# Optimization experiments

Measured on AMD Instinct MI355X. Metric: run time of the kernel, lower is better.

## Reference

```python
import jax, jax.numpy as jnp
import numpy as np

IN_DIM = 1024
FF = 512
OUT = 128
TEMP = 1.0  # temperature=1 passed in __init__
EPS = 1e-5  # BatchNorm3d eps


def make_pe(n, d):
    # PositionalEncoding table, rows 0..n-1
    pos = jnp.arange(n, dtype=jnp.float32)[:, None]
    div = jnp.exp(jnp.arange(0, d, 2, dtype=jnp.float32) * (-np.log(10000.0) / d))
    ang = pos * div  # [n, d/2]
    return jnp.stack([jnp.sin(ang), jnp.cos(ang)], axis=-1).reshape(n, d)


def _nonlocal(x, kw, qw, vw, ow, ob, g, beta):
    # x: [B, C, T, H, W]; 1x1x1 convs are channel matmuls
    B, C, T, H, W = x.shape
    K = jnp.einsum('bcthw,fc->bfthw', x, kw).reshape(B, FF, -1)
    Q = jnp.einsum('bcthw,fc->bfthw', x, qw).reshape(B, FF, -1)
    V = jnp.einsum('bcthw,fc->bfthw', x, vw).reshape(B, FF, -1)
    KQ = jnp.einsum('bcn,bcm->bnm', K, Q)  # K^T Q over channels -> [B,N,N]
    attn = jax.nn.softmax(KQ / TEMP, axis=2)
    # torch: sum_j V[b,c,n] * attn[b,n,j]  == V * attn.sum(axis=2)
    Vo = (V * attn.sum(axis=2)[:, None, :]).reshape(B, FF, T, H, W)
    o = jnp.einsum('bfthw,of->bothw', Vo, ow) + ob[None, :, None, None, None]
    y = x + jax.nn.relu(o)
    # BatchNorm3d, training-mode batch statistics over (B,T,H,W)
    m = y.mean(axis=(0, 2, 3, 4))
    v = y.var(axis=(0, 2, 3, 4))
    inv = jax.lax.rsqrt(v + EPS)
    return ((y - m[None, :, None, None, None]) * inv[None, :, None, None, None]
            * g[None, :, None, None, None] + beta[None, :, None, None, None])


def _convt2(x, w, b):
    # ConvTranspose2d(kernel=2, stride=2): each input pixel emits a 2x2 block
    B, C, H, W = x.shape
    y = jnp.einsum('bchw,cokl->bohkwl', x, w).reshape(B, w.shape[1], 2 * H, 2 * W)
    return y + b[None, :, None, None]


def setup_inputs() -> dict:
    key = jax.random.key(0)
    ks = jax.random.split(key, 32)
    n = lambda k, s, sc: jax.random.normal(k, s, dtype=jnp.float32) * sc
    d = {
        'context': n(ks[0], (4, 4, IN_DIM, 16, 16), 1.0),
        'frame': n(ks[1], (4, 6, IN_DIM, 8, 8), 1.0),
    }
    i = 2
    for l in (0, 1):
        d[f'nl{l}_kw'] = n(ks[i], (FF, IN_DIM), IN_DIM ** -0.5); i += 1
        d[f'nl{l}_qw'] = n(ks[i], (FF, IN_DIM), IN_DIM ** -0.5); i += 1
        d[f'nl{l}_vw'] = n(ks[i], (FF, IN_DIM), IN_DIM ** -0.5); i += 1
        d[f'nl{l}_ow'] = n(ks[i], (IN_DIM, FF), FF ** -0.5); i += 1
        d[f'nl{l}_ob'] = n(ks[i], (IN_DIM,), 0.02); i += 1
        d[f'nl{l}_g'] = jnp.ones((IN_DIM,), jnp.float32)
        d[f'nl{l}_beta'] = jnp.zeros((IN_DIM,), jnp.float32)
    d['tp_w'] = n(ks[i], (FF, IN_DIM, 3, 3, 3), (IN_DIM * 27) ** -0.5); i += 1
    d['tp_b'] = n(ks[i], (FF,), 0.02); i += 1
    d['up1_w'] = n(ks[i], (IN_DIM, FF, 2, 2), IN_DIM ** -0.5); i += 1
    d['up1_b'] = n(ks[i], (FF,), 0.02); i += 1
    d['up2_w'] = n(ks[i], (FF, FF, 2, 2), FF ** -0.5); i += 1
    d['up2_b'] = n(ks[i], (FF,), 0.02); i += 1
    for p in ('og', 'os'):
        d[f'{p}1_w'] = n(ks[i], (FF, FF), FF ** -0.5); i += 1
        d[f'{p}1_b'] = n(ks[i], (FF,), 0.02); i += 1
        d[f'{p}2_w'] = n(ks[i], (OUT, FF), FF ** -0.5); i += 1
        d[f'{p}2_b'] = n(ks[i], (OUT,), 0.02); i += 1
    return d


def reference(context, frame,
              nl0_kw, nl0_qw, nl0_vw, nl0_ow, nl0_ob, nl0_g, nl0_beta,
              nl1_kw, nl1_qw, nl1_vw, nl1_ow, nl1_ob, nl1_g, nl1_beta,
              tp_w, tp_b, up1_w, up1_b, up2_w, up2_b,
              og1_w, og1_b, og2_w, og2_b, os1_w, os1_b, os2_w, os2_b):
    # context: [B, Tc, C, H, W] -> [B, C, Tc, H, W]
    x = jnp.transpose(context, (0, 2, 1, 3, 4))
    x = _nonlocal(x, nl0_kw, nl0_qw, nl0_vw, nl0_ow, nl0_ob, nl0_g, nl0_beta)
    x = _nonlocal(x, nl1_kw, nl1_qw, nl1_vw, nl1_ow, nl1_ob, nl1_g, nl1_beta)
    # temporal pool: Conv3d kernel 3, VALID, then ReLU and global avg pool
    tp = jax.lax.conv_general_dilated(x, tp_w, (1, 1, 1), 'VALID',
                                      dimension_numbers=('NCDHW', 'OIDHW', 'NCDHW'))
    tp = jax.nn.relu(tp + tp_b[None, :, None, None, None])
    goal_pre = tp.mean(axis=(2, 3, 4))  # [B, FF]
    B, T, C, H, W = frame.shape
    f = frame.reshape(B * T, C, H, W)
    s = jax.nn.relu(_convt2(f, up1_w, up1_b))
    s = _convt2(s, up2_w, up2_b)  # [B*T, FF, 4H, 4W]
    Ns = 16 * H * W
    se = s.reshape(B * T, FF, Ns)
    pe = make_pe(Ns, FF)
    Vt = jnp.transpose(se, (0, 2, 1)) + pe[None]  # [B*T, Ns, FF]
    goal_rep = jnp.repeat(goal_pre, T, axis=0)  # [B*T, FF]
    SG = jnp.einsum('bcn,bc->bn', se, goal_rep)
    attn = jax.nn.softmax(SG / TEMP, axis=1)
    sga = jnp.einsum('bn,bnc->bc', attn, Vt).reshape(B, T, FF)
    goal = jax.nn.relu(goal_pre @ og1_w.T + og1_b) @ og2_w.T + og2_b
    state = jax.nn.relu(sga @ os1_w.T + os1_b) @ os2_w.T + os2_b
    return goal, state
```

## Files before the change

kernel.cpp:

```cpp
#include <hip/hip_runtime.h>
#include <hip/hip_bf16.h>

using bf16 = __hip_bfloat16;
typedef short short8 __attribute__((ext_vector_type(8)));
typedef float float4v __attribute__((ext_vector_type(4)));

__device__ __forceinline__ float b2f(unsigned short u){
  unsigned int x = ((unsigned int)u) << 16; float f;
  __builtin_memcpy(&f, &x, 4); return f;
}
__device__ __forceinline__ float b2f(bf16 v){ return __bfloat162float(v); }
__device__ __forceinline__ unsigned short f2bu(float x){
  bf16 h = __float2bfloat16(x); unsigned short u;
  __builtin_memcpy(&u, &h, 2); return u;
}

#define GLDS16(g, l) __builtin_amdgcn_global_load_lds( \
    (const __attribute__((address_space(1))) void*)(g), \
    (__attribute__((address_space(3))) void*)(l), 16, 0, 0)

template<int N> __device__ __forceinline__ void vwait(){
  if constexpr (N==0)       asm volatile("s_waitcnt vmcnt(0)" ::: "memory");
  else if constexpr (N==3)  asm volatile("s_waitcnt vmcnt(3)" ::: "memory");
  else if constexpr (N==4)  asm volatile("s_waitcnt vmcnt(4)" ::: "memory");
  else if constexpr (N==5)  asm volatile("s_waitcnt vmcnt(5)" ::: "memory");
  else if constexpr (N==6)  asm volatile("s_waitcnt vmcnt(6)" ::: "memory");
  else if constexpr (N==8)  asm volatile("s_waitcnt vmcnt(8)" ::: "memory");
  else if constexpr (N==10) asm volatile("s_waitcnt vmcnt(10)" ::: "memory");
  else                      asm volatile("s_waitcnt vmcnt(12)" ::: "memory");
}

template<class TO>
__launch_bounds__(256)
__global__ void permT_k(const float* __restrict__ inp, TO* __restrict__ outp,
                        int Cc, int R, int D, int G, long inS, long outS){
  __shared__ float t[64][65];
  int z = blockIdx.z;
  const float* in = inp + (size_t)z*inS;
  TO* out = outp + (size_t)z*outS;
  int c0 = blockIdx.x*64, r0 = blockIdx.y*64;
  int tid = threadIdx.x;
  int rr = tid>>2, c4 = (tid&3)*16;
  const float* p = in + (size_t)(r0+rr)*Cc + c0 + c4;
  #pragma unroll
  for (int j=0;j<16;j+=4){
    float4 q = *reinterpret_cast<const float4*>(p+j);
    t[rr][c4+j]=q.x; t[rr][c4+j+1]=q.y; t[rr][c4+j+2]=q.z; t[rr][c4+j+3]=q.w;
  }
  __syncthreads();
  int ql = tid>>2;
  int q = c0 + ql;
  int orow = (q % D)*G + q / D;
  TO* op = out + (size_t)orow*R + r0 + c4;
  #pragma unroll
  for (int j=0;j<16;j++){
    if constexpr (sizeof(TO)==2) op[j] = __float2bfloat16(t[c4+j][ql]);
    else op[j] = t[c4+j][ql];
  }
}

template<int PAT>
__launch_bounds__(256)
__global__ void permTsplit3_k(const float* __restrict__ inp, unsigned short* __restrict__ outp,
                              int Cc, int R, int D, int G, long inS, long outS){
  __shared__ float t[64][65];
  int z = blockIdx.z;
  const float* in = inp + (size_t)z*inS;
  unsigned short* out = outp + (size_t)z*outS;
  int c0 = blockIdx.x*64, r0 = blockIdx.y*64;
  int tid = threadIdx.x;
  int rr = tid>>2, c4 = (tid&3)*16;
  const float* p = in + (size_t)(r0+rr)*Cc + c0 + c4;
  #pragma unroll
  for (int j=0;j<16;j+=4){
    float4 q = *reinterpret_cast<const float4*>(p+j);
    t[rr][c4+j]=q.x; t[rr][c4+j+1]=q.y; t[rr][c4+j+2]=q.z; t[rr][c4+j+3]=q.w;
  }
  __syncthreads();
  int ql = tid>>2;
  int q = c0 + ql;
  int orow = (q % D)*G + q / D;
  unsigned short* op = out + (size_t)orow*(3*R);
  #pragma unroll
  for (int j=0;j<16;j++){
    float v = t[c4+j][ql];
    unsigned short h = f2bu(v);
    unsigned short l = f2bu(v - b2f(h));
    int idx = r0 + c4 + j;
    if constexpr (PAT==0){
      op[idx] = h; op[R+idx] = l; op[2*R+idx] = h;
    } else {
      op[idx] = h; op[R+idx] = h; op[2*R+idx] = l;
    }
  }
}

__launch_bounds__(256)
__global__ void splitA_k(const float* __restrict__ in, unsigned short* __restrict__ out){
  int idx = blockIdx.x*256 + threadIdx.x;
  int m = idx >> 9, j = idx & 511;
  float v = in[idx];
  unsigned short h = f2bu(v);
  unsigned short l = f2bu(v - b2f(h));
  unsigned short* op = out + (size_t)m*1536 + j;
  op[0] = h; op[512] = l; op[1024] = h;
}

__global__ void zero_k(float* __restrict__ p){
  p[blockIdx.x*256 + threadIdx.x] = 0.f;
}

template<int WM, int WN, int MTM, int NTN, int MODE, int BK>
__launch_bounds__(256)
__global__ void mmL_k(const unsigned short* __restrict__ A,
                      const unsigned short* __restrict__ B,
                      const float* __restrict__ bias,
                      const unsigned short* __restrict__ res,
                      const float* __restrict__ gpf,
                      float* __restrict__ outf,
                      unsigned short* __restrict__ outs,
                      float* __restrict__ aux,
                      int K){
  constexpr int BM  = WM*MTM*16;
  constexpr int BN  = WN*NTN*16;
  constexpr int CPR = BK/8;
  constexpr int KS  = BK/32;
  constexpr int AIT = (BM*CPR)/256;
  constexpr int NBC = (BN*CPR)/256;
  constexpr int LPT = AIT + NBC;
  __shared__ __align__(16) short As[3*BM*BK];
  __shared__ __align__(16) short Bs[3*BN*BK];
  const int tid = threadIdx.x;
  const int wv = tid>>6, lane = tid&63, l15 = lane&15, quad = lane>>4;
  const int wvm = wv / WN, wvf = wv % WN;
  const int wbase = wv<<6;

  int bx = blockIdx.x, by = blockIdx.y, bz = blockIdx.z;
  if constexpr (MODE==1){
    const int gx = gridDim.x, gy = gridDim.y, gz = gridDim.z;
    const int n = gx*gy*gz;
    const int lin = bx + gx*(by + gy*bz);
    const int q = n >> 3, r = n & 7;
    const int xcd = lin & 7, j = lin >> 3;
    const int work = (xcd < r ? xcd*(q+1) : r*(q+1) + (xcd-r)*q) + j;
    by = work % gy;
    const int t = work / gy;
    bx = t % gx;
    bz = t / gx;
  }
  const int m0 = bx*BM;
  const int fblk = by*BN;
  const int z = bz;

  auto swz = [](int row){ if constexpr (BK==32) return (row>>1)&3; else return row&7; };

  size_t aAddr[AIT];
  #pragma unroll
  for (int it=0; it<AIT; ++it){
    int s = tid + it*256;
    int arow = s/CPR;
    int ac = (s&(CPR-1)) ^ swz(arow);
    int m = m0 + arow;
    if constexpr (MODE==1){
      int mm = m < 1568 ? m : 1567;
      int b = mm/392, r = mm%392;
      int t = r/196, r2 = r%196;
      int hh = r2/14, ww = r2%14;
      int kt = z/3, kh = z%3;
      int sp = ((b*4 + t + kt)*16 + hh + kh)*16 + ww;
      aAddr[it] = (size_t)sp*1024 + ac*8;
    } else {
      aAddr[it] = (size_t)m*K + ac*8;
    }
  }
  size_t bAddr[NBC];
  #pragma unroll
  for (int it=0; it<NBC; ++it){
    int s = tid + it*256;
    int row = s/CPR;
    int c = (s&(CPR-1)) ^ swz(row);
    int f = fblk + row;
    if constexpr (MODE==0)      bAddr[it] = (size_t)f*1024 + c*8;
    else if constexpr (MODE==1) bAddr[it] = (size_t)f*27648 + (size_t)z*3072 + c*8;
    else                        bAddr[it] = ((size_t)z*512 + f)*(size_t)K + c*8;
  }
  int aslot[MTM][KS];
  #pragma unroll
  for (int mt=0;mt<MTM;++mt)
    #pragma unroll
    for (int ks=0;ks<KS;++ks){
      int row = wvm*MTM*16 + mt*16 + l15;
      aslot[mt][ks] = row*CPR + ((ks*4 + quad) ^ swz(row));
    }
  int bslot[NTN][KS];
  #pragma unroll
  for (int nt=0;nt<NTN;++nt)
    #pragma unroll
    for (int ks=0;ks<KS;++ks){
      int row = wvf*NTN*16 + nt*16 + l15;
      bslot[nt][ks] = row*CPR + ((ks*4 + quad) ^ swz(row));
    }

  float4v acc[MTM][NTN];
  #pragma unroll
  for (int i=0;i<MTM;i++)
    #pragma unroll
    for (int j=0;j<NTN;j++) acc[i][j]=(float4v){0,0,0,0};

  auto stage = [&](int buf, int k0){
    #pragma unroll
    for (int it=0; it<AIT; ++it)
      GLDS16(A + aAddr[it] + k0, As + buf*(BM*BK) + (it*256 + wbase)*8);
    #pragma unroll
    for (int it=0; it<NBC; ++it)
      GLDS16(B + bAddr[it] + k0, Bs + buf*(BN*BK) + (it*256 + wbase)*8);
  };
  auto computeTile = [&](int buf){
    const short* ap = As + buf*(BM*BK);
    const short* bp = Bs + buf*(BN*BK);
    #pragma unroll
    for (int ks=0; ks<KS; ++ks){
      short8 bf[NTN];
      #pragma unroll
      for (int nt=0;nt<NTN;++nt)
        bf[nt] = *reinterpret_cast<const short8*>(bp + bslot[nt][ks]*8);
      #pragma unroll
      for (int mt=0;mt<MTM;++mt){
        short8 af = *reinterpret_cast<const short8*>(ap + aslot[mt][ks]*8);
        #pragma unroll
        for (int nt=0;nt<NTN;++nt)
          acc[mt][nt] = __builtin_amdgcn_mfma_f32_16x16x32_bf16(af, bf[nt], acc[mt][nt],0,0,0);
      }
    }
  };

  const int nt = K/BK;
  int b0=0, b1=1, b2=2;
  stage(b0, 0);
  for (int t=0; t<nt-1; ++t){
    stage(b1, (t+1)*BK);
    vwait<LPT>();
    __builtin_amdgcn_sched_barrier(0);
    __builtin_amdgcn_s_barrier();
    __builtin_amdgcn_sched_barrier(0);
    computeTile(b0);
    int tmp=b0; b0=b1; b1=b2; b2=tmp;
  }
  vwait<0>();
  __builtin_amdgcn_sched_barrier(0);
  __builtin_amdgcn_s_barrier();
  __builtin_amdgcn_sched_barrier(0);
  computeTile(b0);

  if constexpr (MODE==0){
    const float* badd = outf;
    float sacc[NTN] = {}, s2acc[NTN] = {};
    #pragma unroll
    for (int nt2=0;nt2<NTN;++nt2){
      int f = fblk + wvf*NTN*16 + nt2*16 + l15;
      float bi = bias[f] + (badd ? badd[f] : 0.f);
      float rsc = 1.f, rsh = 0.f;
      if (gpf){ rsc = gpf[f]; rsh = gpf[1024+f]; }
      #pragma unroll
      for (int mt=0;mt<MTM;++mt){
        #pragma unroll
        for (int r=0;r<4;++r){
          int m = m0 + wvm*MTM*16 + mt*16 + quad*4 + r;
          float v = fmaxf(acc[mt][nt2][r]+bi, 0.f) + b2f(res[(size_t)m*1024 + f])*rsc + rsh;
          outs[(size_t)m*1024 + f] = f2bu(v);
          sacc[nt2] += v; s2acc[nt2] += v*v;
        }
      }
    }
    #pragma unroll
    for (int nt2=0;nt2<NTN;++nt2){
      float s = sacc[nt2], s2 = s2acc[nt2];
      s  += __shfl_xor(s, 16);  s  += __shfl_xor(s, 32);
      s2 += __shfl_xor(s2, 16); s2 += __shfl_xor(s2, 32);
      if (quad==0){
        int f = fblk + wvf*NTN*16 + nt2*16 + l15;
        aux[(size_t)bx*2048 + f] = s;
        aux[(size_t)bx*2048 + 1024 + f] = s2;
      }
    }
  } else if constexpr (MODE==1){
    #pragma unroll
    for (int mt=0;mt<MTM;++mt)
      #pragma unroll
      for (int nt2=0;nt2<NTN;++nt2){
        int f = fblk + wvf*NTN*16 + nt2*16 + l15;
        #pragma unroll
        for (int r=0;r<4;++r){
          int m = m0 + wvm*MTM*16 + mt*16 + quad*4 + r;
          if (m < 1568) outf[((size_t)z*1568 + m)*512 + f] = acc[mt][nt2][r];
        }
      }
  } else if constexpr (MODE==2){
    int kk = z>>1, ll = z&1;
    #pragma unroll
    for (int mt=0;mt<MTM;++mt)
      #pragma unroll
      for (int nt2=0;nt2<NTN;++nt2){
        int f = fblk + wvf*NTN*16 + nt2*16 + l15;
        float bi = bias[f];
        #pragma unroll
        for (int r=0;r<4;++r){
          int m = m0 + wvm*MTM*16 + mt*16 + quad*4 + r;
          int bt = m>>6, p = m&63;
          long orow = (long)bt*256 + (2*(p>>3)+kk)*16 + 2*(p&7)+ll;
          float v = fmaxf(acc[mt][nt2][r]+bi, 0.f);
          unsigned short h = f2bu(v);
          unsigned short l = f2bu(v - b2f(h));
          unsigned short* rp = outs + (size_t)orow*1536 + f;
          rp[0] = h; rp[512] = l; rp[1024] = h;
        }
      }
  } else if constexpr (MODE==5){
    int kk = z>>1, ll = z&1;
    #pragma unroll
    for (int mt=0;mt<MTM;++mt){
      int mbase = m0 + wvm*MTM*16 + mt*16;
      int bt = mbase>>8, b6 = bt/6, p0 = mbase&255;
      float gv[NTN], bv[NTN];
      #pragma unroll
      for (int nt2=0;nt2<NTN;++nt2){
        int f = fblk + wvf*NTN*16 + nt2*16 + l15;
        gv[nt2] = gpf[b6*512 + f];
        bv[nt2] = bias[f];
      }
      #pragma unroll
      for (int r=0;r<4;++r){
        int p = p0 + quad*4 + r;
        long orow = (long)bt*1024 + (2*(p>>4)+kk)*32 + 2*(p&15)+ll;
        float sdot = 0.f;
        #pragma unroll
        for (int nt2=0;nt2<NTN;++nt2){
          int f = fblk + wvf*NTN*16 + nt2*16 + l15;
          float v = acc[mt][nt2][r] + bv[nt2];
          outf[(size_t)orow*512 + f] = v;
          sdot += v * gv[nt2];
        }
        sdot += __shfl_xor(sdot, 1); sdot += __shfl_xor(sdot, 2);
        sdot += __shfl_xor(sdot, 4); sdot += __shfl_xor(sdot, 8);
        if (l15==0) atomicAdd(aux + orow, sdot);
      }
    }
  } else {
    if (gpf){
      float sc[NTN], sh[NTN];
      #pragma unroll
      for (int nt2=0;nt2<NTN;++nt2){
        int f = fblk + wvf*NTN*16 + nt2*16 + l15;
        sc[nt2] = gpf[f]; sh[nt2] = gpf[1024+f];
      }
      #pragma unroll
      for (int mt=0;mt<MTM;++mt){
        #pragma unroll
        for (int r=0;r<4;++r){
          int m = m0 + wvm*MTM*16 + mt*16 + quad*4 + r;
          float part = 0.f;
          #pragma unroll
          for (int nt2=0;nt2<NTN;++nt2){
            int f = fblk + wvf*NTN*16 + nt2*16 + l15;
            float a = acc[mt][nt2][r];
            part += a * sh[nt2];
            outs[(size_t)m*1024 + f] = f2bu(a * sc[nt2]);
          }
          part += __shfl_xor(part, 1); part += __shfl_xor(part, 2);
          part += __shfl_xor(part, 4); part += __shfl_xor(part, 8);
          if (l15==0) atomicAdd(aux + m, part);
        }
      }
    } else {
      #pragma unroll
      for (int mt=0;mt<MTM;++mt)
        #pragma unroll
        for (int nt2=0;nt2<NTN;++nt2){
          int f = fblk + wvf*NTN*16 + nt2*16 + l15;
          #pragma unroll
          for (int r=0;r<4;++r){
            int m = m0 + wvm*MTM*16 + mt*16 + quad*4 + r;
            outs[(size_t)m*1024 + f] = f2bu(acc[mt][nt2][r]);
          }
        }
    }
  }
}

__global__ void stats_comb(const float* __restrict__ bnp, const float* __restrict__ g,
                           const float* __restrict__ beta, float* __restrict__ mv){
  int c = blockIdx.x*256 + threadIdx.x;
  float S=0.f, S2=0.f;
  #pragma unroll 8
  for (int s=0;s<64;s++){ S += bnp[(size_t)s*2048 + c]; S2 += bnp[(size_t)s*2048 + 1024 + c]; }
  float m = S * (1.f/4096.f);
  float var = S2 * (1.f/4096.f) - m*m;
  float inv = rsqrtf(var + 1e-5f);
  float sc = inv * g[c];
  mv[c] = sc;
  mv[1024 + c] = beta[c] - m*sc;
}

__launch_bounds__(256)
__global__ void wperm_k(const float* __restrict__ w, const float* __restrict__ mv1,
                        unsigned short* __restrict__ wtt, float* __restrict__ tpb2){
  __shared__ float ls[3456];
  __shared__ float rs[256];
  int f = blockIdx.x, cc = blockIdx.y;
  const float* src = w + (size_t)f*27648 + cc*3456;
  unsigned short* dst = wtt + (size_t)f*27648;
  for (int i=threadIdx.x; i<3456; i+=256) ls[i] = src[i];
  __syncthreads();
  float part = 0.f;
  for (int u=threadIdx.x; u<3456; u+=256){
    int j = u >> 7, c = u & 127;
    int ch = cc*128 + c;
    float wv = ls[c*27 + j];
    dst[(size_t)j*1024 + ch] = f2bu(wv * mv1[ch]);
    part += wv * mv1[1024 + ch];
  }
  rs[threadIdx.x] = part; __syncthreads();
  for (int st=128; st>0; st>>=1){
    if (threadIdx.x < st) rs[threadIdx.x] += rs[threadIdx.x+st];
    __syncthreads();
  }
  if (threadIdx.x==0) atomicAdd(tpb2 + f, rs[0]);
}

__launch_bounds__(256)
__global__ void gp2_k(const float* __restrict__ part9, const float* __restrict__ tpb,
                      const float* __restrict__ tpbA, float* __restrict__ gp){
  int b = blockIdx.x;
  int fc = blockIdx.y;
  int z = blockIdx.z;
  int fi = threadIdx.x & 31, pi = threadIdx.x >> 5;
  int f = fc*32 + fi;
  float bias = tpb[f] + tpbA[f];
  float a = 0.f;
  for (int p = z*49 + pi; p < z*49 + 49; p += 8){
    size_t base = ((size_t)(b*392 + p))*512 + f;
    float v = bias;
    #pragma unroll
    for (int i=0;i<9;i++) v += part9[(size_t)i*802816 + base];
    a += fmaxf(v, 0.f);
  }
  __shared__ float red[256];
  red[threadIdx.x] = a; __syncthreads();
  for (int st=4; st>0; st>>=1){
    if (pi < st) red[pi*32+fi] += red[(pi+st)*32+fi];
    __syncthreads();
  }
  if (pi==0) atomicAdd(gp + b*512 + f, red[fi] * (1.f/392.f));
}

__global__ void pen_k(float* __restrict__ peN){
  int idx = blockIdx.x*256 + threadIdx.x;
  int n = idx >> 9, c = idx & 511;
  float div = expf(-0.035977892f * (float)(c>>1));
  float ang = (float)n * div;
  peN[idx] = (c & 1) ? cosf(ang) : sinf(ang);
}

__launch_bounds__(256)
__global__ void softmax_k(const float* __restrict__ SG, float* __restrict__ attn){
  int bt = blockIdx.x; int tid = threadIdx.x;
  float4 v = *reinterpret_cast<const float4*>(SG + bt*1024 + tid*4);
  float mx = fmaxf(fmaxf(v.x,v.y), fmaxf(v.z,v.w));
  __shared__ float red[256];
  red[tid] = mx; __syncthreads();
  for (int st=128; st>0; st>>=1){
    if (tid<st) red[tid] = fmaxf(red[tid], red[tid+st]);
    __syncthreads();
  }
  float m = red[0]; __syncthreads();
  float4 e;
  e.x = expf(v.x-m); e.y = expf(v.y-m); e.z = expf(v.z-m); e.w = expf(v.w-m);
  red[tid] = e.x+e.y+e.z+e.w; __syncthreads();
  for (int st=128; st>0; st>>=1){
    if (tid<st) red[tid] += red[tid+st];
    __syncthreads();
  }
  float inv = 1.0f/red[0];
  e.x*=inv; e.y*=inv; e.z*=inv; e.w*=inv;
  *reinterpret_cast<float4*>(attn + bt*1024 + tid*4) = e;
}

__launch_bounds__(256)
__global__ void sga2_k(const float* __restrict__ scl, const float* __restrict__ peN,
                       const float* __restrict__ attn, float* __restrict__ sga){
  int bt = blockIdx.x, sl = blockIdx.y;
  int tid = threadIdx.x;
  __shared__ float at[32];
  if (tid < 32) at[tid] = attn[bt*1024 + sl*32 + tid];
  __syncthreads();
  float acc0 = 0.f, acc1 = 0.f;
  for (int j=0;j<32;j++){
    int n = sl*32 + j;
    float a = at[j];
    const float* row = scl + ((size_t)bt*1024 + n)*512;
    const float* pe  = peN + (size_t)n*512;
    acc0 += a * (row[tid] + pe[tid]);
    acc1 += a * (row[tid+256] + pe[tid+256]);
  }
  atomicAdd(sga + (size_t)bt*512 + tid, acc0);
  atomicAdd(sga + (size_t)bt*512 + 256 + tid, acc1);
}

__launch_bounds__(256)
__global__ void mlp_k(const float* __restrict__ in, const float* __restrict__ w1,
                      const float* __restrict__ b1, const float* __restrict__ w2,
                      const float* __restrict__ b2, float* __restrict__ out){
  int bb = blockIdx.x; int tid = threadIdx.x;
  __shared__ float xv[512]; __shared__ float h[512];
  xv[tid] = in[(size_t)bb*512 + tid];
  xv[tid+256] = in[(size_t)bb*512 + 256 + tid];
  __syncthreads();
  #pragma unroll
  for (int oo=0;oo<2;oo++){
    int o = tid + oo*256;
    const float* wr = w1 + (size_t)o*512;
    float a=0.f;
    for (int c=0;c<512;c+=4){
      float4 q = *reinterpret_cast<const float4*>(wr+c);
      a += xv[c]*q.x + xv[c+1]*q.y + xv[c+2]*q.z + xv[c+3]*q.w;
    }
    h[o] = fmaxf(a + b1[o], 0.f);
  }
  __syncthreads();
  if (tid < 128){
    const float* wr = w2 + (size_t)tid*512;
    float a=0.f;
    for (int c=0;c<512;c+=4){
      float4 q = *reinterpret_cast<const float4*>(wr+c);
      a += h[c]*q.x + h[c+1]*q.y + h[c+2]*q.z + h[c+3]*q.w;
    }
    out[(size_t)bb*128+tid] = a + b2[tid];
  }
}

extern "C" void kernel_launch(void* const* d_in, const int* in_sizes, int n_in,
                              void* d_out, int out_size, void* d_ws, size_t ws_size,
                              hipStream_t stream){
  (void)in_sizes; (void)n_in; (void)out_size; (void)ws_size;
  const float* ctx   = (const float*)d_in[0];
  const float* frame = (const float*)d_in[1];
  const float* nl_vw[2] = {(const float*)d_in[4],  (const float*)d_in[11]};
  const float* nl_ow[2] = {(const float*)d_in[5],  (const float*)d_in[12]};
  const float* nl_ob[2] = {(const float*)d_in[6],  (const float*)d_in[13]};
  const float* nl_g[2]  = {(const float*)d_in[7],  (const float*)d_in[14]};
  const float* nl_be[2] = {(const float*)d_in[8],  (const float*)d_in[15]};
  const float* tp_w = (const float*)d_in[16]; const float* tp_b = (const float*)d_in[17];
  const float* up1w = (const float*)d_in[18]; const float* up1b = (const float*)d_in[19];
  const float* up2w = (const float*)d_in[20]; const float* up2b = (const float*)d_in[21];
  const float* og1w = (const float*)d_in[22]; const float* og1b = (const float*)d_in[23];
  const float* og2w = (const float*)d_in[24]; const float* og2b = (const float*)d_in[25];
  const float* os1w = (const float*)d_in[26]; const float* os1b = (const float*)d_in[27];
  const float* os2w = (const float*)d_in[28]; const float* os2b = (const float*)d_in[29];
  float* out = (float*)d_out;

  char* wsp = (char*)d_ws;
  float* bias2   = (float*)(wsp + 65536);
  float* tpb2    = (float*)(wsp + 69632);
  float* gp      = (float*)(wsp + 73728);
  float* mv0     = (float*)(wsp + 131072);
  float* mv1     = (float*)(wsp + 139264);
  float* SG      = (float*)(wsp + 147456);
  float* attn    = (float*)(wsp + 245760);
  float* sga     = (float*)(wsp + 344064);
  float* peN     = (float*)(wsp + 786432);
  bf16*  weff    = (bf16*) (wsp + 2883584);
  unsigned short* w1sp = (unsigned short*)(wsp + 4980736);
  unsigned short* w2sp = (unsigned short*)(wsp + 17563648);
  char* ov = wsp + 23855104;
  bf16*  xclA = (bf16*) (ov);
  bf16*  xclB = (bf16*) (ov + 8388608);
  unsigned short* Asp = (unsigned short*)(ov + 36700160);
  unsigned short* Bsp = (unsigned short*)(ov + 36700160 + 3145728);
  float* bnp = (float*)(ov + 36700160 + 6291456);
  unsigned short* wtt = (unsigned short*)(ov + 8388608);
  float* part9 = (float*)(ov + 36700160);
  unsigned short* Fsp = (unsigned short*)(ov + 36700160);
  unsigned short* s1sp = (unsigned short*)(ov);
  float* scl  = (float*)(ov + 18874368);

  permT_k<bf16><<<dim3(4,16,16),256,0,stream>>>(ctx, xclA, 256, 1024, 1, 1, 262144L, 262144L);
  permTsplit3_k<1><<<dim3(32,16,1),256,0,stream>>>(up1w, w1sp, 2048, 1024, 4, 512, 0L, 0L);
  permTsplit3_k<1><<<dim3(32,8,1),256,0,stream>>>(up2w, w2sp, 2048, 512, 4, 512, 0L, 0L);
  pen_k<<<2048,256,0,stream>>>(peN);
  zero_k<<<320,256,0,stream>>>((float*)(wsp + 65536));

  splitA_k<<<2048,256,0,stream>>>(nl_ow[0], Asp);
  permTsplit3_k<1><<<dim3(16,8,1),256,0,stream>>>(nl_vw[0], Bsp, 1024, 512, 1, 1, 0L, 0L);
  mmL_k<1,4,2,2,4,64><<<dim3(32,8,1),256,0,stream>>>(Asp, Bsp, nullptr, nullptr, nullptr,
      nullptr, (unsigned short*)weff, nullptr, 1536);
  mmL_k<1,4,4,2,0,64><<<dim3(64,8,1),256,0,stream>>>((const unsigned short*)xclA,
      (const unsigned short*)weff, nl_ob[0], (const unsigned short*)xclA, nullptr,
      nullptr, (unsigned short*)xclB, bnp, 1024);
  stats_comb<<<4,256,0,stream>>>(bnp, nl_g[0], nl_be[0], mv0);

  splitA_k<<<2048,256,0,stream>>>(nl_ow[1], Asp);
  permTsplit3_k<1><<<dim3(16,8,1),256,0,stream>>>(nl_vw[1], Bsp, 1024, 512, 1, 1, 0L, 0L);
  mmL_k<1,4,2,2,4,64><<<dim3(32,8,1),256,0,stream>>>(Asp, Bsp, nullptr, nullptr, mv0,
      nullptr, (unsigned short*)weff, bias2, 1536);
  mmL_k<1,4,4,2,0,64><<<dim3(64,8,1),256,0,stream>>>((const unsigned short*)xclB,
      (const unsigned short*)weff, nl_ob[1], (const unsigned short*)xclB, mv0,
      bias2, (unsigned short*)xclA, bnp, 1024);
  stats_comb<<<4,256,0,stream>>>(bnp, nl_g[1], nl_be[1], mv1);

  wperm_k<<<dim3(512,8),256,0,stream>>>(tp_w, mv1, wtt, tpb2);
  mmL_k<2,2,4,4,1,32><<<dim3(13,4,9),256,0,stream>>>((const unsigned short*)xclA, wtt,
      nullptr, nullptr, nullptr, part9, nullptr, nullptr, 3072);
  gp2_k<<<dim3(4,16,8),256,0,stream>>>(part9, tp_b, tpb2, gp);

  permTsplit3_k<0><<<dim3(1,16,24),256,0,stream>>>(frame, Fsp, 64, 1024, 1, 1, 65536L, 196608L);
  mmL_k<1,4,4,2,2,64><<<dim3(24,4,4),256,0,stream>>>(Fsp, w1sp, up1b, nullptr, nullptr,
      nullptr, s1sp, nullptr, 3072);
  mmL_k<2,2,4,4,5,32><<<dim3(48,4,4),256,0,stream>>>(s1sp, w2sp, up2b, nullptr, gp,
      scl, nullptr, SG, 1536);

  softmax_k<<<24,256,0,stream>>>(SG, attn);
  sga2_k<<<dim3(24,32),256,0,stream>>>(scl, peN, attn, sga);

  mlp_k<<<4,256,0,stream>>>(gp, og1w, og1b, og2w, og2b, out);
  mlp_k<<<24,256,0,stream>>>(sga, os1w, os1b, os2w, os2b, out + 512);
}
```

Measured before the change: 602.8 us.

## Merge prep kernels into combined launches and add 4-buffer pipeline for temporal-pool GEMM

Five independent preprocessing launches (context transpose, two upconv weight splits, positional encoding, zeroing) are merged into one prep kernel that dispatches on block index. The per-layer splitA and value-weight split are merged into one layerprep kernel. This cuts launch overhead and idle gaps between small kernels. The temporal-pool GEMM also gets a 4-buffer LDS pipeline with prefetch distance two, in place of the 3-buffer scheme, to hide more load latency. The cost is more shared memory per block, which may lower occupancy.

```diff
diff --git a/kernel.cpp b/kernel.cpp
--- a/kernel.cpp
+++ b/kernel.cpp
@@ -30,16 +30,12 @@
   else                      asm volatile("s_waitcnt vmcnt(12)" ::: "memory");
 }
 
-template<class TO>
-__launch_bounds__(256)
-__global__ void permT_k(const float* __restrict__ inp, TO* __restrict__ outp,
-                        int Cc, int R, int D, int G, long inS, long outS){
-  __shared__ float t[64][65];
-  int z = blockIdx.z;
-  const float* in = inp + (size_t)z*inS;
-  TO* out = outp + (size_t)z*outS;
-  int c0 = blockIdx.x*64, r0 = blockIdx.y*64;
-  int tid = threadIdx.x;
+__device__ __forceinline__ void permT_body(const float* inp, bf16* outp,
+    int Cc, int R, int D, int G, long inS, long outS,
+    int bx, int by, int bz, int tid, float (*t)[65]){
+  const float* in = inp + (size_t)bz*inS;
+  bf16* out = outp + (size_t)bz*outS;
+  int c0 = bx*64, r0 = by*64;
   int rr = tid>>2, c4 = (tid&3)*16;
   const float* p = in + (size_t)(r0+rr)*Cc + c0 + c4;
   #pragma unroll
@@ -51,24 +47,18 @@
   int ql = tid>>2;
   int q = c0 + ql;
   int orow = (q % D)*G + q / D;
-  TO* op = out + (size_t)orow*R + r0 + c4;
-  #pragma unroll
-  for (int j=0;j<16;j++){
-    if constexpr (sizeof(TO)==2) op[j] = __float2bfloat16(t[c4+j][ql]);
-    else op[j] = t[c4+j][ql];
-  }
+  bf16* op = out + (size_t)orow*R + r0 + c4;
+  #pragma unroll
+  for (int j=0;j<16;j++) op[j] = __float2bfloat16(t[c4+j][ql]);
 }
 
 template<int PAT>
-__launch_bounds__(256)
-__global__ void permTsplit3_k(const float* __restrict__ inp, unsigned short* __restrict__ outp,
-                              int Cc, int R, int D, int G, long inS, long outS){
-  __shared__ float t[64][65];
-  int z = blockIdx.z;
-  const float* in = inp + (size_t)z*inS;
-  unsigned short* out = outp + (size_t)z*outS;
-  int c0 = blockIdx.x*64, r0 = blockIdx.y*64;
-  int tid = threadIdx.x;
+__device__ __forceinline__ void permTsplit3_body(const float* inp, unsigned short* outp,
+    int Cc, int R, int D, int G, long inS, long outS,
+    int bx, int by, int bz, int tid, float (*t)[65]){
+  const float* in = inp + (size_t)bz*inS;
+  unsigned short* out = outp + (size_t)bz*outS;
+  int c0 = bx*64, r0 = by*64;
   int rr = tid>>2, c4 = (tid&3)*16;
   const float* p = in + (size_t)(r0+rr)*Cc + c0 + c4;
   #pragma unroll
@@ -95,9 +85,9 @@
   }
 }
 
-__launch_bounds__(256)
-__global__ void splitA_k(const float* __restrict__ in, unsigned short* __restrict__ out){
-  int idx = blockIdx.x*256 + threadIdx.x;
+__device__ __forceinline__ void splitA_body(const float* in, unsigned short* out,
+                                            int blk, int tid){
+  int idx = blk*256 + tid;
   int m = idx >> 9, j = idx & 511;
   float v = in[idx];
   unsigned short h = f2bu(v);
@@ -106,11 +96,58 @@
   op[0] = h; op[512] = l; op[1024] = h;
 }
 
-__global__ void zero_k(float* __restrict__ p){
-  p[blockIdx.x*256 + threadIdx.x] = 0.f;
-}
-
-template<int WM, int WN, int MTM, int NTN, int MODE, int BK>
+__launch_bounds__(256)
+__global__ void prep_k(const float* __restrict__ ctx, bf16* __restrict__ xclA,
+                       const float* __restrict__ up1w, unsigned short* __restrict__ w1sp,
+                       const float* __restrict__ up2w, unsigned short* __restrict__ w2sp,
+                       float* __restrict__ peN, float* __restrict__ zbase){
+  __shared__ float t[64][65];
+  int b = blockIdx.x, tid = threadIdx.x;
+  if (b < 1024){
+    permT_body(ctx, xclA, 256, 1024, 1, 1, 262144L, 262144L,
+               b&3, (b>>2)&15, b>>6, tid, t);
+  } else if (b < 1536){
+    b -= 1024;
+    permTsplit3_body<1>(up1w, w1sp, 2048, 1024, 4, 512, 0L, 0L,
+                        b&31, b>>5, 0, tid, t);
+  } else if (b < 1792){
+    b -= 1536;
+    permTsplit3_body<1>(up2w, w2sp, 2048, 512, 4, 512, 0L, 0L,
+                        b&31, b>>5, 0, tid, t);
+  } else if (b < 3840){
+    int idx = (b-1792)*256 + tid;
+    int n = idx >> 9, c = idx & 511;
+    float div = expf(-0.035977892f * (float)(c>>1));
+    float ang = (float)n * div;
+    peN[idx] = (c & 1) ? cosf(ang) : sinf(ang);
+  } else {
+    zbase[(b-3840)*256 + tid] = 0.f;
+  }
+}
+
+__launch_bounds__(256)
+__global__ void layerprep_k(const float* __restrict__ ow, unsigned short* __restrict__ Asp,
+                            const float* __restrict__ vw, unsigned short* __restrict__ Bsp){
+  __shared__ float t[64][65];
+  int b = blockIdx.x, tid = threadIdx.x;
+  if (b < 2048){
+    splitA_body(ow, Asp, b, tid);
+  } else {
+    b -= 2048;
+    permTsplit3_body<1>(vw, Bsp, 1024, 512, 1, 1, 0L, 0L, b&15, b>>4, 0, tid, t);
+  }
+}
+
+template<int PAT>
+__launch_bounds__(256)
+__global__ void permTsplit3_k(const float* __restrict__ inp, unsigned short* __restrict__ outp,
+                              int Cc, int R, int D, int G, long inS, long outS){
+  __shared__ float t[64][65];
+  permTsplit3_body<PAT>(inp, outp, Cc, R, D, G, inS, outS,
+                        blockIdx.x, blockIdx.y, blockIdx.z, threadIdx.x, t);
+}
+
+template<int WM, int WN, int MTM, int NTN, int MODE, int BK, int NBUF=3>
 __launch_bounds__(256)
 __global__ void mmL_k(const unsigned short* __restrict__ A,
                       const unsigned short* __restrict__ B,
@@ -128,8 +165,8 @@
   constexpr int AIT = (BM*CPR)/256;
   constexpr int NBC = (BN*CPR)/256;
   constexpr int LPT = AIT + NBC;
-  __shared__ __align__(16) short As[3*BM*BK];
-  __shared__ __align__(16) short Bs[3*BN*BK];
+  __shared__ __align__(16) short As[NBUF*BM*BK];
+  __shared__ __align__(16) short Bs[NBUF*BN*BK];
   const int tid = threadIdx.x;
   const int wv = tid>>6, lane = tid&63, l15 = lane&15, quad = lane>>4;
   const int wvm = wv / WN, wvf = wv % WN;
@@ -235,22 +272,37 @@
   };
 
   const int nt = K/BK;
-  int b0=0, b1=1, b2=2;
-  stage(b0, 0);
-  for (int t=0; t<nt-1; ++t){
-    stage(b1, (t+1)*BK);
-    vwait<LPT>();
+  if constexpr (NBUF==3){
+    int b0=0, b1=1, b2=2;
+    stage(b0, 0);
+    for (int t=0; t<nt-1; ++t){
+      stage(b1, (t+1)*BK);
+      vwait<LPT>();
+      __builtin_amdgcn_sched_barrier(0);
+      __builtin_amdgcn_s_barrier();
+      __builtin_amdgcn_sched_barrier(0);
+      computeTile(b0);
+      int tmp=b0; b0=b1; b1=b2; b2=tmp;
+    }
+    vwait<0>();
     __builtin_amdgcn_sched_barrier(0);
     __builtin_amdgcn_s_barrier();
     __builtin_amdgcn_sched_barrier(0);
     computeTile(b0);
-    int tmp=b0; b0=b1; b1=b2; b2=tmp;
-  }
-  vwait<0>();
-  __builtin_amdgcn_sched_barrier(0);
-  __builtin_amdgcn_s_barrier();
-  __builtin_amdgcn_sched_barrier(0);
-  computeTile(b0);
+  } else {
+    stage(0, 0);
+    stage(1, BK);
+    for (int t=0; t<nt; ++t){
+      if (t+2 < nt) stage((t+2)&3, (t+2)*BK);
+      if (t+2 < nt)      vwait<2*LPT>();
+      else if (t+1 < nt) vwait<LPT>();
+      else               vwait<0>();
+      __builtin_amdgcn_sched_barrier(0);
+      __builtin_amdgcn_s_barrier();
+      __builtin_amdgcn_sched_barrier(0);
+      computeTile(t&3);
+    }
+  }
 
   if constexpr (MODE==0){
     const float* badd = outf;
@@ -451,14 +503,6 @@
     __syncthreads();
   }
   if (pi==0) atomicAdd(gp + b*512 + f, red[fi] * (1.f/392.f));
-}
-
-__global__ void pen_k(float* __restrict__ peN){
-  int idx = blockIdx.x*256 + threadIdx.x;
-  int n = idx >> 9, c = idx & 511;
-  float div = expf(-0.035977892f * (float)(c>>1));
-  float ang = (float)n * div;
-  peN[idx] = (c & 1) ? cosf(ang) : sinf(ang);
 }
 
 __launch_bounds__(256)
@@ -583,14 +627,10 @@
   unsigned short* s1sp = (unsigned short*)(ov);
   float* scl  = (float*)(ov + 18874368);
 
-  permT_k<bf16><<<dim3(4,16,16),256,0,stream>>>(ctx, xclA, 256, 1024, 1, 1, 262144L, 262144L);
-  permTsplit3_k<1><<<dim3(32,16,1),256,0,stream>>>(up1w, w1sp, 2048, 1024, 4, 512, 0L, 0L);
-  permTsplit3_k<1><<<dim3(32,8,1),256,0,stream>>>(up2w, w2sp, 2048, 512, 4, 512, 0L, 0L);
-  pen_k<<<2048,256,0,stream>>>(peN);
-  zero_k<<<320,256,0,stream>>>((float*)(wsp + 65536));
-
-  splitA_k<<<2048,256,0,stream>>>(nl_ow[0], Asp);
-  permTsplit3_k<1><<<dim3(16,8,1),256,0,stream>>>(nl_vw[0], Bsp, 1024, 512, 1, 1, 0L, 0L);
+  prep_k<<<4160,256,0,stream>>>(ctx, xclA, up1w, w1sp, up2w, w2sp, peN,
+                                (float*)(wsp + 65536));
+
+  layerprep_k<<<2176,256,0,stream>>>(nl_ow[0], Asp, nl_vw[0], Bsp);
   mmL_k<1,4,2,2,4,64><<<dim3(32,8,1),256,0,stream>>>(Asp, Bsp, nullptr, nullptr, nullptr,
       nullptr, (unsigned short*)weff, nullptr, 1536);
   mmL_k<1,4,4,2,0,64><<<dim3(64,8,1),256,0,stream>>>((const unsigned short*)xclA,
@@ -598,8 +638,7 @@
       nullptr, (unsigned short*)xclB, bnp, 1024);
   stats_comb<<<4,256,0,stream>>>(bnp, nl_g[0], nl_be[0], mv0);
 
-  splitA_k<<<2048,256,0,stream>>>(nl_ow[1], Asp);
-  permTsplit3_k<1><<<dim3(16,8,1),256,0,stream>>>(nl_vw[1], Bsp, 1024, 512, 1, 1, 0L, 0L);
+  layerprep_k<<<2176,256,0,stream>>>(nl_ow[1], Asp, nl_vw[1], Bsp);
   mmL_k<1,4,2,2,4,64><<<dim3(32,8,1),256,0,stream>>>(Asp, Bsp, nullptr, nullptr, mv0,
       nullptr, (unsigned short*)weff, bias2, 1536);
   mmL_k<1,4,4,2,0,64><<<dim3(64,8,1),256,0,stream>>>((const unsigned short*)xclB,
@@ -608,7 +647,7 @@
   stats_comb<<<4,256,0,stream>>>(bnp, nl_g[1], nl_be[1], mv1);
 
   wperm_k<<<dim3(512,8),256,0,stream>>>(tp_w, mv1, wtt, tpb2);
-  mmL_k<2,2,4,4,1,32><<<dim3(13,4,9),256,0,stream>>>((const unsigned short*)xclA, wtt,
+  mmL_k<2,2,4,4,1,32,4><<<dim3(13,4,9),256,0,stream>>>((const unsigned short*)xclA, wtt,
       nullptr, nullptr, nullptr, part9, nullptr, nullptr, 3072);
   gp2_k<<<dim3(4,16,8),256,0,stream>>>(part9, tp_b, tpb2, gp);
 
```

Result: faster. 568.5 us (-5.7%).
